# Optimization experiments

Measured on AMD Instinct MI355X. Metric: run time of the kernel, lower is better.

Reference implementation:

```python
import jax, jax.numpy as jnp
import numpy as np

B, L, C, H, W = 4, 8, 32, 128, 256
M1, M2 = 32, 32  # spectral modes


def setup_inputs() -> dict:
    key = jax.random.key(0)
    k1, k2, k3, k4, k5, k6 = jax.random.split(key, 6)
    scale = 1.0 / (C * C)
    return {
        "x": jax.random.normal(k1, (B, L, C, H, W), dtype=jnp.float32),
        "k": jax.random.normal(k2, (C, H, W), dtype=jnp.float32),
        "w1r": scale * jax.random.normal(k3, (C, C, M1, M2), dtype=jnp.float32),
        "w1i": scale * jax.random.normal(k4, (C, C, M1, M2), dtype=jnp.float32),
        "w2r": scale * jax.random.normal(k5, (C, C, M1, M2), dtype=jnp.float32),
        "w2i": scale * jax.random.normal(k6, (C, C, M1, M2), dtype=jnp.float32),
    }


def reference(x, k, w1r, w1i, w2r, w2i):
    # x: [B, L, C, H, W] real; k: [C, H, W] conv kernel (broadcast over B*L).
    b, l, c, h, w = x.shape
    # --- FlashFFTConvInterface fallback path: circular conv via rfft2.
    # H, W are already 2/3/5-smooth (next_fast_len is identity -> no padding).
    u = x.reshape(b * l, c, h, w)
    u_f = jnp.fft.rfft2(u)                     # [B*L, C, H, W//2+1] complex
    k_f = jnp.fft.rfft2(k)                     # [C, H, W//2+1], broadcasts
    y = jnp.fft.irfft2(u_f * k_f, s=(h, w)).reshape(b, l, c, h, w)

    # --- SpectralConv2d: per-mode channel mixing in frequency domain.
    x_f = jnp.fft.rfft2(y)                     # [B, L, C, H, Wf] complex
    wf = x_f.shape[-1]
    w1 = (w1r + 1j * w1i).astype(x_f.dtype)
    w2 = (w2r + 1j * w2i).astype(x_f.dtype)
    m1 = min(h, M1)
    m2 = min(wf, M2)
    co = w1.shape[1]
    top = jnp.einsum('blcij,coij->bloij', x_f[:, :, :, :m1, :m2], w1[:, :, :m1, :m2])
    out_f = jnp.zeros((b, l, co, h, wf), dtype=x_f.dtype)
    out_f = out_f.at[:, :, :, :m1, :m2].set(top)
    if h > 1 and (h > M1 or wf > M2):
        bot = jnp.einsum('blcij,coij->bloij', x_f[:, :, :, h - m1:, :m2], w2[:, :, :m1, :m2])
        out_f = out_f.at[:, :, :, h - m1:, :m2].set(bot)
    return jnp.fft.irfft2(out_f, s=(h, w))    # [B, L, Co, H, W] real
```

## Files before the change

kernel.cpp:

```cpp
#include <hip/hip_runtime.h>
#include <math.h>

#define Hn 128
#define Wn 256
#define PLANE (Hn*Wn)

#define OFF_TQC 0u
#define OFF_TQS 2048u
#define OFF_TP  4096u
#define OFF_KM  16384u
#define OFF_XM  147456u
#define OFF_B   4341760u
#define OFF_RK  12730368u

__global__ __launch_bounds__(256) void build_tables(float* __restrict__ ws) {
  int tid = blockIdx.x * 256 + threadIdx.x;
  const double PI2 = 6.283185307179586476925286766559;
  if (tid < 512) {
    int j = tid >> 4, xi = tid & 15;
    float cc[4], ss[4];
#pragma unroll
    for (int m = 0; m < 4; m++) {
      int x = xi * 4 + m;
      double ang = PI2 * (double)((j * x) & 255) / 256.0;
      cc[m] = (float)cos(ang); ss[m] = (float)sin(ang);
    }
    ((float4*)(ws + OFF_TQC))[tid] = make_float4(cc[0], cc[1], cc[2], cc[3]);
    ((float4*)(ws + OFF_TQS))[tid] = make_float4(ss[0], ss[1], ss[2], ss[3]);
  }
  if (tid < 2048) {
    int p = tid >> 6, y2 = tid & 63;
    double a0 = PI2 * (double)((p * (2 * y2)) & 127) / 128.0;
    double a1 = PI2 * (double)((p * (2 * y2 + 1)) & 127) / 128.0;
    ((float4*)(ws + OFF_TP))[tid] =
        make_float4((float)cos(a0), (float)sin(a0), (float)cos(a1), (float)sin(a1));
  }
}

#define RS 276
__global__ __launch_bounds__(256, 3) void fwd_rows(const float* __restrict__ src,
                                                   float2* __restrict__ R,
                                                   const float* __restrict__ ws) {
  int plane = blockIdx.x >> 2, chunk = blockIdx.x & 3;
  __shared__ __align__(16) float Sd[32 * RS];
  __shared__ float4 Tc[544], Ts[544];
  int t = threadIdx.x;
  const float4* src4 = (const float4*)src;
  size_t sb = (size_t)plane * 8192 + (size_t)chunk * 2048;
#pragma unroll
  for (int k = 0; k < 8; k++) {
    int idx = t + 256 * k;
    int row = idx >> 6, c4 = idx & 63;
    int sws = (row >> 1) & 15;
    *(float4*)&Sd[row * RS + ((c4 ^ sws) << 2)] = src4[sb + idx];
  }
  const float4* gTc = (const float4*)(ws + OFF_TQC);
  const float4* gTs = (const float4*)(ws + OFF_TQS);
#pragma unroll
  for (int k = 0; k < 2; k++) {
    int idx = t + 256 * k;
    Tc[(idx >> 4) * 17 + (idx & 15)] = gTc[idx];
    Ts[(idx >> 4) * 17 + (idx & 15)] = gTs[idx];
  }
  __syncthreads();
  float EPv[2][4], EMv[2][4], OPv[2][4], OMv[2][4];
  float spE64[2], spU128[2], spO64[2];
#pragma unroll
  for (int uu = 0; uu < 2; uu++) {
    int unit = uu * 256 + t;
    int y = unit >> 4, xq = unit & 15;
    int sws = (y >> 1) & 15;
    const float* rowp = &Sd[y * RS];
    float4 A0 = *(const float4*)&rowp[(xq ^ sws) << 2];
    float4 A2 = *(const float4*)&rowp[((32 + xq) ^ sws) << 2];
    float Av0[4] = {A0.x, A0.y, A0.z, A0.w};
    float Av2[4] = {A2.x, A2.y, A2.z, A2.w};
    float M1[4], M2[4];
#pragma unroll
    for (int kk = 0; kk < 4; kk++) {
      int s1 = 128 - 4 * xq - kk;
      M1[kk] = rowp[(((s1 >> 2) ^ sws) << 2) + (s1 & 3)];
      int s2 = 256 - 4 * xq - kk;
      int s2c = (s2 > 255) ? 255 : s2;
      M2[kk] = rowp[(((s2c >> 2) ^ sws) << 2) + (s2c & 3)];
    }
#pragma unroll
    for (int kk = 0; kk < 4; kk++) {
      float a = Av0[kk] + M2[kk], b = Av0[kk] - M2[kk];
      float c = M1[kk] + Av2[kk], d = M1[kk] - Av2[kk];
      EPv[uu][kk] = a + c;  EMv[uu][kk] = a - c;
      OPv[uu][kk] = b + d;  OMv[uu][kk] = b - d;
    }
    spE64[uu] = 0.f; spU128[uu] = 0.f; spO64[uu] = 0.f;
    if (xq == 0) {
      EPv[uu][0] = Av0[0];  EMv[uu][0] = Av0[0];
      OPv[uu][0] = 0.f;     OMv[uu][0] = 0.f;
      float u64v  = rowp[((16 ^ sws) << 2)];
      float u192v = rowp[((48 ^ sws) << 2)];
      spE64[uu]  = u64v + u192v;
      spO64[uu]  = u64v - u192v;
      spU128[uu] = Av2[0];
    }
  }
  __syncthreads();
#pragma unroll
  for (int uu = 0; uu < 2; uu++) {
    int unit = uu * 256 + t;
    int y = unit >> 4, xq = unit & 15;
    int sws = (y >> 1) & 15;
    float* rowp = &Sd[y * RS];
    int off = (xq ^ sws) << 2;
    *(float4*)&rowp[off]       = make_float4(EPv[uu][0], EPv[uu][1], EPv[uu][2], EPv[uu][3]);
    *(float4*)&rowp[68 + off]  = make_float4(EMv[uu][0], EMv[uu][1], EMv[uu][2], EMv[uu][3]);
    *(float4*)&rowp[136 + off] = make_float4(OMv[uu][0], OMv[uu][1], OMv[uu][2], OMv[uu][3]);
    *(float4*)&rowp[204 + off] = make_float4(OPv[uu][0], OPv[uu][1], OPv[uu][2], OPv[uu][3]);
    if (xq == 0) {
      rowp[64] = spE64[uu];
      rowp[65] = spU128[uu];
      rowp[66] = spO64[uu];
    }
  }
  __syncthreads();
  int jg = t & 15, yg = t >> 4;
  int jodd = jg & 1;
  int aC = jodd ? 68 : 0;
  int aS = jodd ? 204 : 136;
  const float4* pC0 = &Tc[jg * 17];
  const float4* pS0 = &Ts[jg * 17];
  const float4* pC1 = &Tc[(jg + 16) * 17];
  const float4* pS1 = &Ts[(jg + 16) * 17];
  float sgE = jodd ? 0.f : (((jg >> 1) & 1) ? -1.f : 1.f);
  float sgO = jodd ? ((((jg - 1) >> 1) & 1) ? -1.f : 1.f) : 0.f;
  float pm = jodd ? -1.f : 1.f;
  int sw = yg;
  const float* row0 = &Sd[(2 * yg) * RS];
  const float* row1 = &Sd[(2 * yg + 1) * RS];
  float dc[2][2], dsn[2][2];
#pragma unroll
  for (int a = 0; a < 2; a++)
#pragma unroll
    for (int b = 0; b < 2; b++) { dc[a][b] = 0.f; dsn[a][b] = 0.f; }
#define DOT4(a, b) (a.x * b.x + a.y * b.y + a.z * b.z + a.w * b.w)
#pragma unroll 4
  for (int xb = 0; xb < 16; xb++) {
    int off = (xb ^ sw) << 2;
    float4 eY0 = *(const float4*)&row0[aC + off];
    float4 eY1 = *(const float4*)&row1[aC + off];
    float4 oY0 = *(const float4*)&row0[aS + off];
    float4 oY1 = *(const float4*)&row1[aS + off];
    float4 c0 = pC0[xb], s0 = pS0[xb];
    float4 c1 = pC1[xb], s1 = pS1[xb];
    dc[0][0] += DOT4(eY0, c0);  dc[0][1] += DOT4(eY1, c0);
    dc[1][0] += DOT4(eY0, c1);  dc[1][1] += DOT4(eY1, c1);
    dsn[0][0] += DOT4(oY0, s0); dsn[0][1] += DOT4(oY1, s0);
    dsn[1][0] += DOT4(oY0, s1); dsn[1][1] += DOT4(oY1, s1);
  }
#undef DOT4
  float E64_0 = row0[64], u128_0 = row0[65], O64_0 = row0[66];
  float E64_1 = row1[64], u128_1 = row1[65], O64_1 = row1[66];
#pragma unroll
  for (int jj = 0; jj < 2; jj++) {
    int j = jg + 16 * jj;
#pragma unroll
    for (int ky = 0; ky < 2; ky++) {
      int y = chunk * 32 + yg * 2 + ky;
      float E64 = ky ? E64_1 : E64_0;
      float u128 = ky ? u128_1 : u128_0;
      float O64 = ky ? O64_1 : O64_0;
      float re = dc[jj][ky] + sgE * E64 + pm * u128;
      float im = -dsn[jj][ky] - sgO * O64;
      R[((size_t)plane * 128 + y) * 32 + j] = make_float2(re, im);
    }
  }
}
#undef RS

__global__ __launch_bounds__(256) void fwd_cols(const float2* __restrict__ Rg,
                                                float2* __restrict__ dst,
                                                const float* __restrict__ ws) {
  int plane = blockIdx.x;
  __shared__ float4 Rs4[2048];
  __shared__ float4 TPs[2048];
  float2* Rs = (float2*)Rs4;
  int t = threadIdx.x;
  const float4* in4 = (const float4*)(Rg + (size_t)plane * 4096);
#pragma unroll
  for (int k = 0; k < 8; k++) Rs4[t + 256 * k] = in4[t + 256 * k];
  const float4* gTP = (const float4*)(ws + OFF_TP);
#pragma unroll
  for (int k = 0; k < 8; k++) TPs[t + 256 * k] = gTP[t + 256 * k];
  __syncthreads();
  int j = t & 31, pg = t >> 5;
  float Are[4], Aim[4], Bre[4], Bim[4];
#pragma unroll
  for (int m = 0; m < 4; m++) { Are[m] = Aim[m] = Bre[m] = Bim[m] = 0.f; }
  for (int it = 0; it < 32; it++) {
#pragma unroll
    for (int h = 0; h < 2; h++) {
      int y2 = 2 * it + h;
      float sg = (h == 0) ? 1.f : -1.f;
      float2 r0 = Rs[(2 * y2) * 32 + j];
      float2 r1 = Rs[(2 * y2 + 1) * 32 + j];
#pragma unroll
      for (int m = 0; m < 4; m++) {
        int p = pg + 8 * m;
        float4 tw = TPs[p * 64 + y2];
        float P0 = r0.x * tw.x + r0.y * tw.y;
        float Q0 = r0.y * tw.x - r0.x * tw.y;
        float P1 = r1.x * tw.z + r1.y * tw.w;
        float Q1 = r1.y * tw.z - r1.x * tw.w;
        Are[m] += P0 + P1;
        Aim[m] += Q0 + Q1;
        Bre[m] += sg * (P0 - Q1);
        Bim[m] += sg * (Q0 + P1);
      }
    }
  }
  size_t ob = (size_t)plane * 2048;
#pragma unroll
  for (int m = 0; m < 4; m++) {
    int p = pg + 8 * m;
    dst[ob + p * 32 + j] = make_float2(Are[m], Aim[m]);
    dst[ob + (32 + p) * 32 + j] = make_float2(Bre[m], Bim[m]);
  }
}

__global__ __launch_bounds__(256) void wk_build(const float* __restrict__ w1r,
                                                const float* __restrict__ w1i,
                                                const float* __restrict__ w2r,
                                                const float* __restrict__ w2i,
                                                float2* __restrict__ wk,
                                                const float2* __restrict__ km) {
  int e0 = blockIdx.x * 256 + threadIdx.x;
#pragma unroll
  for (int k = 0; k < 4; k++) {
    int e = e0 + k * 524288;
    int o = e & 31, c = (e >> 5) & 31, j = (e >> 10) & 31, i64 = e >> 15;
    int r = (i64 < 32) ? i64 : i64 - 32;
    const float* wr = (i64 < 32) ? w1r : w2r;
    const float* wi = (i64 < 32) ? w1i : w2i;
    int widx = ((c * 32 + o) * 32 + r) * 32 + j;
    float wrv = wr[widx], wiv = wi[widx];
    float2 kv = km[(size_t)c * 2048 + i64 * 32 + j];
    wk[e] = make_float2(kv.x * wrv - kv.y * wiv, kv.x * wiv + kv.y * wrv);
  }
}

__global__ __launch_bounds__(256) void mix_modes(float2* __restrict__ xm,
                                                 const float2* __restrict__ wk) {
  int bid = blockIdx.x;
  int mode = (bid & 7) * 256 + (bid >> 3);
  __shared__ float4 Xs4[512], Ws4[512];
  float2* Xs = (float2*)Xs4;
  float2* Wsl = (float2*)Ws4;
  int t = threadIdx.x;
#pragma unroll
  for (int k = 0; k < 4; k++) {
    int p = t + 256 * k;
    Xs[p] = xm[(size_t)p * 2048 + mode];
  }
  const float4* wk4 = (const float4*)(wk + (size_t)mode * 1024);
#pragma unroll
  for (int k = 0; k < 2; k++) Ws4[t + 256 * k] = wk4[t + 256 * k];
  __syncthreads();
  int o = t & 31, bg = t >> 5;
  float orr[4], oii[4];
#pragma unroll
  for (int m = 0; m < 4; m++) { orr[m] = 0.f; oii[m] = 0.f; }
  for (int c2 = 0; c2 < 16; c2++) {
    float2 w0 = Wsl[(2 * c2) * 32 + o];
    float2 w1 = Wsl[(2 * c2 + 1) * 32 + o];
#pragma unroll
    for (int m = 0; m < 4; m++) {
      float4 xv = *(const float4*)&Xs[(bg * 4 + m) * 32 + 2 * c2];
      orr[m] += xv.x * w0.x - xv.y * w0.y + xv.z * w1.x - xv.w * w1.y;
      oii[m] += xv.x * w0.y + xv.y * w0.x + xv.z * w1.y + xv.w * w1.x;
    }
  }
#pragma unroll
  for (int m = 0; m < 4; m++)
    xm[(size_t)((bg * 4 + m) * 32 + o) * 2048 + mode] = make_float2(orr[m], oii[m]);
}

__global__ __launch_bounds__(256) void inv_rows(const float2* __restrict__ om,
                                                float2* __restrict__ G,
                                                const float* __restrict__ ws) {
  int plane = blockIdx.x;
  __shared__ float4 Os4[1024];
  __shared__ float4 TPs[2048];
  float2* Os = (float2*)Os4;
  int t = threadIdx.x;
  const float4* in4 = (const float4*)(om + (size_t)plane * 2048);
#pragma unroll
  for (int k = 0; k < 4; k++) Os4[t + 256 * k] = in4[t + 256 * k];
  const float4* gTP = (const float4*)(ws + OFF_TP);
#pragma unroll
  for (int k = 0; k < 8; k++) TPs[t + 256 * k] = gTP[t + 256 * k];
  __syncthreads();
  int j = t & 31, yg = t >> 5;
  float gr[16], gi[16];
#pragma unroll
  for (int k = 0; k < 16; k++) { gr[k] = 0.f; gi[k] = 0.f; }
  for (int p = 0; p < 32; p++) {
    float2 A = Os[p * 32 + j];
    float2 B = Os[(32 + p) * 32 + j];
#pragma unroll
    for (int mp = 0; mp < 8; mp++) {
      int y2 = yg * 8 + mp;
      float4 tw = TPs[p * 64 + y2];
      float sg = ((mp & 1) == 0) ? 1.f : -1.f;
      float Sr = A.x + sg * B.x, Si = A.y + sg * B.y;
      gr[2 * mp]     += Sr * tw.x - Si * tw.y;
      gi[2 * mp]     += Sr * tw.y + Si * tw.x;
      float Tr = A.x + sg * B.y, Ti = A.y - sg * B.x;
      gr[2 * mp + 1] += Tr * tw.z - Ti * tw.w;
      gi[2 * mp + 1] += Tr * tw.w + Ti * tw.z;
    }
  }
  const float inv = 1.0f / 32768.0f;
  size_t gb = (size_t)plane * 128;
#pragma unroll
  for (int mm = 0; mm < 16; mm++) {
    int y = yg * 16 + mm;
    float sr = (j == 0) ? gr[mm] * inv : 2.f * inv * gr[mm];
    float si = (j == 0) ? 0.f : 2.f * inv * gi[mm];
    G[(gb + y) * 32 + j] = make_float2(sr, si);
  }
}

__global__ __launch_bounds__(256) void inv_cols(const float2* __restrict__ G,
                                                float* __restrict__ out,
                                                const float* __restrict__ ws) {
  int plane = blockIdx.x >> 2, chunk = blockIdx.x & 3;
  __shared__ float2 Gs[32 * 33];
  __shared__ float4 Tc[544], Ts[544];
  int t = threadIdx.x;
  const float2* in = G + (size_t)plane * 4096 + (size_t)chunk * 1024;
#pragma unroll
  for (int k = 0; k < 4; k++) {
    int idx = t + 256 * k;
    Gs[(idx >> 5) * 33 + (idx & 31)] = in[idx];
  }
  const float4* gTc = (const float4*)(ws + OFF_TQC);
  const float4* gTs = (const float4*)(ws + OFF_TQS);
#pragma unroll
  for (int k = 0; k < 2; k++) {
    int idx = t + 256 * k;
    Tc[(idx >> 4) * 17 + (idx & 15)] = gTc[idx];
    Ts[(idx >> 4) * 17 + (idx & 15)] = gTs[idx];
  }
  __syncthreads();
  int xi = t & 15, yg = t >> 4;
  float4 Ce[2], Co[2], Se[2], So[2];
  float c64[2], s64[2];
#pragma unroll
  for (int ky = 0; ky < 2; ky++) {
    Ce[ky] = make_float4(0.f, 0.f, 0.f, 0.f);
    Co[ky] = make_float4(0.f, 0.f, 0.f, 0.f);
    Se[ky] = make_float4(0.f, 0.f, 0.f, 0.f);
    So[ky] = make_float4(0.f, 0.f, 0.f, 0.f);
    c64[ky] = 0.f; s64[ky] = 0.f;
  }
#define FMA4(acc, s, v) do { acc.x += (s) * (v).x; acc.y += (s) * (v).y; \
                             acc.z += (s) * (v).z; acc.w += (s) * (v).w; } while (0)
#pragma unroll 4
  for (int jh = 0; jh < 16; jh++) {
    float4 ce = Tc[(2 * jh) * 17 + xi],     se = Ts[(2 * jh) * 17 + xi];
    float4 co = Tc[(2 * jh + 1) * 17 + xi], so = Ts[(2 * jh + 1) * 17 + xi];
    float sgn = (jh & 1) ? -1.f : 1.f;
#pragma unroll
    for (int ky = 0; ky < 2; ky++) {
      float2 ge = Gs[(yg * 2 + ky) * 33 + 2 * jh];
      float2 go = Gs[(yg * 2 + ky) * 33 + 2 * jh + 1];
      FMA4(Ce[ky], ge.x, ce);
      FMA4(Se[ky], ge.y, se);
      FMA4(Co[ky], go.x, co);
      FMA4(So[ky], go.y, so);
      c64[ky] += sgn * ge.x;
      s64[ky] += sgn * go.y;
    }
  }
#undef FMA4
  float* outp = out + (size_t)plane * PLANE + (size_t)chunk * 32 * Wn;
#pragma unroll
  for (int ky = 0; ky < 2; ky++) {
    int y = yg * 2 + ky;
    float* ro = outp + y * Wn;
    float4 C  = make_float4(Ce[ky].x + Co[ky].x, Ce[ky].y + Co[ky].y,
                            Ce[ky].z + Co[ky].z, Ce[ky].w + Co[ky].w);
    float4 Cm = make_float4(Ce[ky].x - Co[ky].x, Ce[ky].y - Co[ky].y,
                            Ce[ky].z - Co[ky].z, Ce[ky].w - Co[ky].w);
    float4 S  = make_float4(Se[ky].x + So[ky].x, Se[ky].y + So[ky].y,
                            Se[ky].z + So[ky].z, Se[ky].w + So[ky].w);
    float4 Sm = make_float4(So[ky].x - Se[ky].x, So[ky].y - Se[ky].y,
                            So[ky].z - Se[ky].z, So[ky].w - Se[ky].w);
    *(float4*)(ro + 4 * xi) =
        make_float4(C.x - S.x, C.y - S.y, C.z - S.z, C.w - S.w);
    *(float4*)(ro + 128 + 4 * xi) =
        make_float4(Cm.x + Sm.x, Cm.y + Sm.y, Cm.z + Sm.z, Cm.w + Sm.w);
    int mb = 128 - 4 * xi;
    ro[mb]     = Cm.x - Sm.x;
    ro[mb - 1] = Cm.y - Sm.y;
    ro[mb - 2] = Cm.z - Sm.z;
    ro[mb - 3] = Cm.w - Sm.w;
    int nb = 256 - 4 * xi;
    if (xi) ro[nb] = C.x + S.x;
    ro[nb - 1] = C.y + S.y;
    ro[nb - 2] = C.z + S.z;
    ro[nb - 3] = C.w + S.w;
    if (xi == 0) {
      ro[64]  = c64[ky] - s64[ky];
      ro[192] = c64[ky] + s64[ky];
    }
  }
}

extern "C" void kernel_launch(void* const* d_in, const int* in_sizes, int n_in,
                              void* d_out, int out_size, void* d_ws, size_t ws_size,
                              hipStream_t stream) {
  (void)in_sizes; (void)n_in; (void)out_size; (void)ws_size;
  const float* x   = (const float*)d_in[0];
  const float* kk  = (const float*)d_in[1];
  const float* w1r = (const float*)d_in[2];
  const float* w1i = (const float*)d_in[3];
  const float* w2r = (const float*)d_in[4];
  const float* w2i = (const float*)d_in[5];
  float*  ws   = (float*)d_ws;
  float*  out  = (float*)d_out;
  float2* km2  = (float2*)(ws + OFF_KM);
  float2* xm2  = (float2*)(ws + OFF_XM);
  float2* bx   = (float2*)(ws + OFF_B);
  float2* rk   = (float2*)(ws + OFF_RK);

  build_tables<<<8, 256, 0, stream>>>(ws);
  fwd_rows<<<4096, 256, 0, stream>>>(x, bx, ws);
  fwd_rows<<<128, 256, 0, stream>>>(kk, rk, ws);
  fwd_cols<<<1024, 256, 0, stream>>>(bx, xm2, ws);
  fwd_cols<<<32, 256, 0, stream>>>(rk, km2, ws);
  wk_build<<<2048, 256, 0, stream>>>(w1r, w1i, w2r, w2i, bx, km2);
  mix_modes<<<2048, 256, 0, stream>>>(xm2, bx);
  inv_rows<<<1024, 256, 0, stream>>>(xm2, bx, ws);
  inv_cols<<<4096, 256, 0, stream>>>(bx, out, ws);
}
```

Measured before the change: 417.9 us.

## Fuse row and column DFT passes into single per-plane forward and inverse kernels

Merges fwd_rows+fwd_cols into one kernel per plane that loops over four row chunks and keeps the 128x32 row-spectrum in LDS, and likewise fuses inv_rows+inv_cols keeping the intermediate in LDS. This removes the global round-trip of intermediate spectra and two launches per direction. Twiddle tables are now read from global/cache instead of staged in LDS, and grids shrink to one block per plane (1024 blocks) with lower occupancy target, which reduces parallelism and may raise latency.

```diff
diff --git a/kernel.cpp b/kernel.cpp
--- a/kernel.cpp
+++ b/kernel.cpp
@@ -38,154 +38,139 @@
 }
 
 #define RS 276
-__global__ __launch_bounds__(256, 3) void fwd_rows(const float* __restrict__ src,
-                                                   float2* __restrict__ R,
-                                                   const float* __restrict__ ws) {
-  int plane = blockIdx.x >> 2, chunk = blockIdx.x & 3;
-  __shared__ __align__(16) float Sd[32 * RS];
-  __shared__ float4 Tc[544], Ts[544];
+__global__ __launch_bounds__(256, 2) void fwd_fused(const float* __restrict__ src,
+                                                    float2* __restrict__ dst,
+                                                    const float* __restrict__ ws) {
+  int plane = blockIdx.x;
+  __shared__ __align__(16) float U[32 * RS];
+  __shared__ __align__(16) float2 RL[128 * 33];
   int t = threadIdx.x;
   const float4* src4 = (const float4*)src;
-  size_t sb = (size_t)plane * 8192 + (size_t)chunk * 2048;
-#pragma unroll
-  for (int k = 0; k < 8; k++) {
-    int idx = t + 256 * k;
-    int row = idx >> 6, c4 = idx & 63;
-    int sws = (row >> 1) & 15;
-    *(float4*)&Sd[row * RS + ((c4 ^ sws) << 2)] = src4[sb + idx];
-  }
+  size_t sb = (size_t)plane * 8192;
   const float4* gTc = (const float4*)(ws + OFF_TQC);
   const float4* gTs = (const float4*)(ws + OFF_TQS);
-#pragma unroll
-  for (int k = 0; k < 2; k++) {
-    int idx = t + 256 * k;
-    Tc[(idx >> 4) * 17 + (idx & 15)] = gTc[idx];
-    Ts[(idx >> 4) * 17 + (idx & 15)] = gTs[idx];
-  }
-  __syncthreads();
-  float EPv[2][4], EMv[2][4], OPv[2][4], OMv[2][4];
-  float spE64[2], spU128[2], spO64[2];
-#pragma unroll
-  for (int uu = 0; uu < 2; uu++) {
-    int unit = uu * 256 + t;
-    int y = unit >> 4, xq = unit & 15;
-    int sws = (y >> 1) & 15;
-    const float* rowp = &Sd[y * RS];
-    float4 A0 = *(const float4*)&rowp[(xq ^ sws) << 2];
-    float4 A2 = *(const float4*)&rowp[((32 + xq) ^ sws) << 2];
-    float Av0[4] = {A0.x, A0.y, A0.z, A0.w};
-    float Av2[4] = {A2.x, A2.y, A2.z, A2.w};
-    float M1[4], M2[4];
-#pragma unroll
-    for (int kk = 0; kk < 4; kk++) {
-      int s1 = 128 - 4 * xq - kk;
-      M1[kk] = rowp[(((s1 >> 2) ^ sws) << 2) + (s1 & 3)];
-      int s2 = 256 - 4 * xq - kk;
-      int s2c = (s2 > 255) ? 255 : s2;
-      M2[kk] = rowp[(((s2c >> 2) ^ sws) << 2) + (s2c & 3)];
-    }
-#pragma unroll
-    for (int kk = 0; kk < 4; kk++) {
-      float a = Av0[kk] + M2[kk], b = Av0[kk] - M2[kk];
-      float c = M1[kk] + Av2[kk], d = M1[kk] - Av2[kk];
-      EPv[uu][kk] = a + c;  EMv[uu][kk] = a - c;
-      OPv[uu][kk] = b + d;  OMv[uu][kk] = b - d;
-    }
-    spE64[uu] = 0.f; spU128[uu] = 0.f; spO64[uu] = 0.f;
-    if (xq == 0) {
-      EPv[uu][0] = Av0[0];  EMv[uu][0] = Av0[0];
-      OPv[uu][0] = 0.f;     OMv[uu][0] = 0.f;
-      float u64v  = rowp[((16 ^ sws) << 2)];
-      float u192v = rowp[((48 ^ sws) << 2)];
-      spE64[uu]  = u64v + u192v;
-      spO64[uu]  = u64v - u192v;
-      spU128[uu] = Av2[0];
-    }
-  }
-  __syncthreads();
-#pragma unroll
-  for (int uu = 0; uu < 2; uu++) {
-    int unit = uu * 256 + t;
-    int y = unit >> 4, xq = unit & 15;
-    int sws = (y >> 1) & 15;
-    float* rowp = &Sd[y * RS];
-    int off = (xq ^ sws) << 2;
-    *(float4*)&rowp[off]       = make_float4(EPv[uu][0], EPv[uu][1], EPv[uu][2], EPv[uu][3]);
-    *(float4*)&rowp[68 + off]  = make_float4(EMv[uu][0], EMv[uu][1], EMv[uu][2], EMv[uu][3]);
-    *(float4*)&rowp[136 + off] = make_float4(OMv[uu][0], OMv[uu][1], OMv[uu][2], OMv[uu][3]);
-    *(float4*)&rowp[204 + off] = make_float4(OPv[uu][0], OPv[uu][1], OPv[uu][2], OPv[uu][3]);
-    if (xq == 0) {
-      rowp[64] = spE64[uu];
-      rowp[65] = spU128[uu];
-      rowp[66] = spO64[uu];
-    }
-  }
-  __syncthreads();
+
   int jg = t & 15, yg = t >> 4;
   int jodd = jg & 1;
   int aC = jodd ? 68 : 0;
   int aS = jodd ? 204 : 136;
-  const float4* pC0 = &Tc[jg * 17];
-  const float4* pS0 = &Ts[jg * 17];
-  const float4* pC1 = &Tc[(jg + 16) * 17];
-  const float4* pS1 = &Ts[(jg + 16) * 17];
+  const float4* pC0 = gTc + jg * 16;
+  const float4* pS0 = gTs + jg * 16;
+  const float4* pC1 = gTc + (jg + 16) * 16;
+  const float4* pS1 = gTs + (jg + 16) * 16;
   float sgE = jodd ? 0.f : (((jg >> 1) & 1) ? -1.f : 1.f);
   float sgO = jodd ? ((((jg - 1) >> 1) & 1) ? -1.f : 1.f) : 0.f;
   float pm = jodd ? -1.f : 1.f;
   int sw = yg;
-  const float* row0 = &Sd[(2 * yg) * RS];
-  const float* row1 = &Sd[(2 * yg + 1) * RS];
-  float dc[2][2], dsn[2][2];
-#pragma unroll
-  for (int a = 0; a < 2; a++)
-#pragma unroll
-    for (int b = 0; b < 2; b++) { dc[a][b] = 0.f; dsn[a][b] = 0.f; }
+
+  for (int ch = 0; ch < 4; ch++) {
+#pragma unroll
+    for (int k = 0; k < 8; k++) {
+      int idx = t + 256 * k;
+      int row = idx >> 6, c4 = idx & 63;
+      int sws = (row >> 1) & 15;
+      *(float4*)&U[row * RS + ((c4 ^ sws) << 2)] = src4[sb + ch * 2048 + idx];
+    }
+    __syncthreads();
+    float EPv[2][4], EMv[2][4], OPv[2][4], OMv[2][4];
+    float spE64[2], spU128[2], spO64[2];
+#pragma unroll
+    for (int uu = 0; uu < 2; uu++) {
+      int unit = uu * 256 + t;
+      int y = unit >> 4, xq = unit & 15;
+      int sws = (y >> 1) & 15;
+      const float* rowp = &U[y * RS];
+      float4 A0 = *(const float4*)&rowp[(xq ^ sws) << 2];
+      float4 A2 = *(const float4*)&rowp[((32 + xq) ^ sws) << 2];
+      float Av0[4] = {A0.x, A0.y, A0.z, A0.w};
+      float Av2[4] = {A2.x, A2.y, A2.z, A2.w};
+      float M1[4], M2[4];
+#pragma unroll
+      for (int kk = 0; kk < 4; kk++) {
+        int s1 = 128 - 4 * xq - kk;
+        M1[kk] = rowp[(((s1 >> 2) ^ sws) << 2) + (s1 & 3)];
+        int s2 = 256 - 4 * xq - kk;
+        int s2c = (s2 > 255) ? 255 : s2;
+        M2[kk] = rowp[(((s2c >> 2) ^ sws) << 2) + (s2c & 3)];
+      }
+#pragma unroll
+      for (int kk = 0; kk < 4; kk++) {
+        float a = Av0[kk] + M2[kk], b = Av0[kk] - M2[kk];
+        float c = M1[kk] + Av2[kk], d = M1[kk] - Av2[kk];
+        EPv[uu][kk] = a + c;  EMv[uu][kk] = a - c;
+        OPv[uu][kk] = b + d;  OMv[uu][kk] = b - d;
+      }
+      spE64[uu] = 0.f; spU128[uu] = 0.f; spO64[uu] = 0.f;
+      if (xq == 0) {
+        EPv[uu][0] = Av0[0];  EMv[uu][0] = Av0[0];
+        OPv[uu][0] = 0.f;     OMv[uu][0] = 0.f;
+        float u64v  = rowp[((16 ^ sws) << 2)];
+        float u192v = rowp[((48 ^ sws) << 2)];
+        spE64[uu]  = u64v + u192v;
+        spO64[uu]  = u64v - u192v;
+        spU128[uu] = Av2[0];
+      }
+    }
+    __syncthreads();
+#pragma unroll
+    for (int uu = 0; uu < 2; uu++) {
+      int unit = uu * 256 + t;
+      int y = unit >> 4, xq = unit & 15;
+      int sws = (y >> 1) & 15;
+      float* rowp = &U[y * RS];
+      int off = (xq ^ sws) << 2;
+      *(float4*)&rowp[off]       = make_float4(EPv[uu][0], EPv[uu][1], EPv[uu][2], EPv[uu][3]);
+      *(float4*)&rowp[68 + off]  = make_float4(EMv[uu][0], EMv[uu][1], EMv[uu][2], EMv[uu][3]);
+      *(float4*)&rowp[136 + off] = make_float4(OMv[uu][0], OMv[uu][1], OMv[uu][2], OMv[uu][3]);
+      *(float4*)&rowp[204 + off] = make_float4(OPv[uu][0], OPv[uu][1], OPv[uu][2], OPv[uu][3]);
+      if (xq == 0) {
+        rowp[64] = spE64[uu];
+        rowp[65] = spU128[uu];
+        rowp[66] = spO64[uu];
+      }
+    }
+    __syncthreads();
+    const float* row0 = &U[(2 * yg) * RS];
+    const float* row1 = &U[(2 * yg + 1) * RS];
+    float dc[2][2], dsn[2][2];
+#pragma unroll
+    for (int a = 0; a < 2; a++)
+#pragma unroll
+      for (int b = 0; b < 2; b++) { dc[a][b] = 0.f; dsn[a][b] = 0.f; }
 #define DOT4(a, b) (a.x * b.x + a.y * b.y + a.z * b.z + a.w * b.w)
 #pragma unroll 4
-  for (int xb = 0; xb < 16; xb++) {
-    int off = (xb ^ sw) << 2;
-    float4 eY0 = *(const float4*)&row0[aC + off];
-    float4 eY1 = *(const float4*)&row1[aC + off];
-    float4 oY0 = *(const float4*)&row0[aS + off];
-    float4 oY1 = *(const float4*)&row1[aS + off];
-    float4 c0 = pC0[xb], s0 = pS0[xb];
-    float4 c1 = pC1[xb], s1 = pS1[xb];
-    dc[0][0] += DOT4(eY0, c0);  dc[0][1] += DOT4(eY1, c0);
-    dc[1][0] += DOT4(eY0, c1);  dc[1][1] += DOT4(eY1, c1);
-    dsn[0][0] += DOT4(oY0, s0); dsn[0][1] += DOT4(oY1, s0);
-    dsn[1][0] += DOT4(oY0, s1); dsn[1][1] += DOT4(oY1, s1);
-  }
+    for (int xb = 0; xb < 16; xb++) {
+      int off = (xb ^ sw) << 2;
+      float4 eY0 = *(const float4*)&row0[aC + off];
+      float4 eY1 = *(const float4*)&row1[aC + off];
+      float4 oY0 = *(const float4*)&row0[aS + off];
+      float4 oY1 = *(const float4*)&row1[aS + off];
+      float4 c0 = pC0[xb], s0 = pS0[xb];
+      float4 c1 = pC1[xb], s1 = pS1[xb];
+      dc[0][0] += DOT4(eY0, c0);  dc[0][1] += DOT4(eY1, c0);
+      dc[1][0] += DOT4(eY0, c1);  dc[1][1] += DOT4(eY1, c1);
+      dsn[0][0] += DOT4(oY0, s0); dsn[0][1] += DOT4(oY1, s0);
+      dsn[1][0] += DOT4(oY0, s1); dsn[1][1] += DOT4(oY1, s1);
+    }
 #undef DOT4
-  float E64_0 = row0[64], u128_0 = row0[65], O64_0 = row0[66];
-  float E64_1 = row1[64], u128_1 = row1[65], O64_1 = row1[66];
-#pragma unroll
-  for (int jj = 0; jj < 2; jj++) {
-    int j = jg + 16 * jj;
-#pragma unroll
-    for (int ky = 0; ky < 2; ky++) {
-      int y = chunk * 32 + yg * 2 + ky;
-      float E64 = ky ? E64_1 : E64_0;
-      float u128 = ky ? u128_1 : u128_0;
-      float O64 = ky ? O64_1 : O64_0;
-      float re = dc[jj][ky] + sgE * E64 + pm * u128;
-      float im = -dsn[jj][ky] - sgO * O64;
-      R[((size_t)plane * 128 + y) * 32 + j] = make_float2(re, im);
-    }
-  }
-}
-#undef RS
-
-__global__ __launch_bounds__(256) void fwd_cols(const float2* __restrict__ Rg,
-                                                float2* __restrict__ dst,
-                                                const float* __restrict__ ws) {
-  int plane = blockIdx.x;
-  __shared__ float4 Rs4[2048];
-  __shared__ float4 TPs[2048];
-  float2* Rs = (float2*)Rs4;
-  int t = threadIdx.x;
-  const float4* in4 = (const float4*)(Rg + (size_t)plane * 4096);
-#pragma unroll
-  for (int k = 0; k < 8; k++) Rs4[t + 256 * k] = in4[t + 256 * k];
+    float E64_0 = row0[64], u128_0 = row0[65], O64_0 = row0[66];
+    float E64_1 = row1[64], u128_1 = row1[65], O64_1 = row1[66];
+#pragma unroll
+    for (int jj = 0; jj < 2; jj++) {
+#pragma unroll
+      for (int ky = 0; ky < 2; ky++) {
+        float E64 = ky ? E64_1 : E64_0;
+        float u128 = ky ? u128_1 : u128_0;
+        float O64 = ky ? O64_1 : O64_0;
+        float re = dc[jj][ky] + sgE * E64 + pm * u128;
+        float im = -dsn[jj][ky] - sgO * O64;
+        RL[(ch * 32 + yg * 2 + ky) * 33 + (jg + 16 * jj)] = make_float2(re, im);
+      }
+    }
+    __syncthreads();
+  }
+
+  float4* TPs = (float4*)U;
   const float4* gTP = (const float4*)(ws + OFF_TP);
 #pragma unroll
   for (int k = 0; k < 8; k++) TPs[t + 256 * k] = gTP[t + 256 * k];
@@ -199,8 +184,8 @@
     for (int h = 0; h < 2; h++) {
       int y2 = 2 * it + h;
       float sg = (h == 0) ? 1.f : -1.f;
-      float2 r0 = Rs[(2 * y2) * 32 + j];
-      float2 r1 = Rs[(2 * y2 + 1) * 32 + j];
+      float2 r0 = RL[(2 * y2) * 33 + j];
+      float2 r1 = RL[(2 * y2 + 1) * 33 + j];
 #pragma unroll
       for (int m = 0; m < 4; m++) {
         int p = pg + 8 * m;
@@ -224,6 +209,7 @@
     dst[ob + (32 + p) * 32 + j] = make_float2(Bre[m], Bim[m]);
   }
 }
+#undef RS
 
 __global__ __launch_bounds__(256) void wk_build(const float* __restrict__ w1r,
                                                 const float* __restrict__ w1i,
@@ -282,135 +268,115 @@
     xm[(size_t)((bg * 4 + m) * 32 + o) * 2048 + mode] = make_float2(orr[m], oii[m]);
 }
 
-__global__ __launch_bounds__(256) void inv_rows(const float2* __restrict__ om,
-                                                float2* __restrict__ G,
-                                                const float* __restrict__ ws) {
+__global__ __launch_bounds__(256, 2) void inv_fused(const float2* __restrict__ om,
+                                                    float* __restrict__ out,
+                                                    const float* __restrict__ ws) {
   int plane = blockIdx.x;
-  __shared__ float4 Os4[1024];
-  __shared__ float4 TPs[2048];
-  float2* Os = (float2*)Os4;
+  __shared__ __align__(16) float4 TPs[2048];
+  __shared__ __align__(16) float2 GL[128 * 33];
   int t = threadIdx.x;
-  const float4* in4 = (const float4*)(om + (size_t)plane * 2048);
-#pragma unroll
-  for (int k = 0; k < 4; k++) Os4[t + 256 * k] = in4[t + 256 * k];
   const float4* gTP = (const float4*)(ws + OFF_TP);
 #pragma unroll
   for (int k = 0; k < 8; k++) TPs[t + 256 * k] = gTP[t + 256 * k];
   __syncthreads();
-  int j = t & 31, yg = t >> 5;
-  float gr[16], gi[16];
-#pragma unroll
-  for (int k = 0; k < 16; k++) { gr[k] = 0.f; gi[k] = 0.f; }
-  for (int p = 0; p < 32; p++) {
-    float2 A = Os[p * 32 + j];
-    float2 B = Os[(32 + p) * 32 + j];
-#pragma unroll
-    for (int mp = 0; mp < 8; mp++) {
-      int y2 = yg * 8 + mp;
-      float4 tw = TPs[p * 64 + y2];
-      float sg = ((mp & 1) == 0) ? 1.f : -1.f;
-      float Sr = A.x + sg * B.x, Si = A.y + sg * B.y;
-      gr[2 * mp]     += Sr * tw.x - Si * tw.y;
-      gi[2 * mp]     += Sr * tw.y + Si * tw.x;
-      float Tr = A.x + sg * B.y, Ti = A.y - sg * B.x;
-      gr[2 * mp + 1] += Tr * tw.z - Ti * tw.w;
-      gi[2 * mp + 1] += Tr * tw.w + Ti * tw.z;
-    }
-  }
-  const float inv = 1.0f / 32768.0f;
-  size_t gb = (size_t)plane * 128;
-#pragma unroll
-  for (int mm = 0; mm < 16; mm++) {
-    int y = yg * 16 + mm;
-    float sr = (j == 0) ? gr[mm] * inv : 2.f * inv * gr[mm];
-    float si = (j == 0) ? 0.f : 2.f * inv * gi[mm];
-    G[(gb + y) * 32 + j] = make_float2(sr, si);
-  }
-}
-
-__global__ __launch_bounds__(256) void inv_cols(const float2* __restrict__ G,
-                                                float* __restrict__ out,
-                                                const float* __restrict__ ws) {
-  int plane = blockIdx.x >> 2, chunk = blockIdx.x & 3;
-  __shared__ float2 Gs[32 * 33];
-  __shared__ float4 Tc[544], Ts[544];
-  int t = threadIdx.x;
-  const float2* in = G + (size_t)plane * 4096 + (size_t)chunk * 1024;
-#pragma unroll
-  for (int k = 0; k < 4; k++) {
-    int idx = t + 256 * k;
-    Gs[(idx >> 5) * 33 + (idx & 31)] = in[idx];
-  }
+  {
+    int j = t & 31, yg = t >> 5;
+    const float2* omp = om + (size_t)plane * 2048;
+    float gr[16], gi[16];
+#pragma unroll
+    for (int k = 0; k < 16; k++) { gr[k] = 0.f; gi[k] = 0.f; }
+    for (int p = 0; p < 32; p++) {
+      float2 A = omp[p * 32 + j];
+      float2 B = omp[(32 + p) * 32 + j];
+#pragma unroll
+      for (int mp = 0; mp < 8; mp++) {
+        int y2 = yg * 8 + mp;
+        float4 tw = TPs[p * 64 + y2];
+        float sg = ((mp & 1) == 0) ? 1.f : -1.f;
+        float Sr = A.x + sg * B.x, Si = A.y + sg * B.y;
+        gr[2 * mp]     += Sr * tw.x - Si * tw.y;
+        gi[2 * mp]     += Sr * tw.y + Si * tw.x;
+        float Tr = A.x + sg * B.y, Ti = A.y - sg * B.x;
+        gr[2 * mp + 1] += Tr * tw.z - Ti * tw.w;
+        gi[2 * mp + 1] += Tr * tw.w + Ti * tw.z;
+      }
+    }
+    const float inv = 1.0f / 32768.0f;
+#pragma unroll
+    for (int mm = 0; mm < 16; mm++) {
+      int y = yg * 16 + mm;
+      float sr = (j == 0) ? gr[mm] * inv : 2.f * inv * gr[mm];
+      float si = (j == 0) ? 0.f : 2.f * inv * gi[mm];
+      GL[y * 33 + j] = make_float2(sr, si);
+    }
+  }
+  __syncthreads();
   const float4* gTc = (const float4*)(ws + OFF_TQC);
   const float4* gTs = (const float4*)(ws + OFF_TQS);
-#pragma unroll
-  for (int k = 0; k < 2; k++) {
-    int idx = t + 256 * k;
-    Tc[(idx >> 4) * 17 + (idx & 15)] = gTc[idx];
-    Ts[(idx >> 4) * 17 + (idx & 15)] = gTs[idx];
-  }
-  __syncthreads();
   int xi = t & 15, yg = t >> 4;
-  float4 Ce[2], Co[2], Se[2], So[2];
-  float c64[2], s64[2];
-#pragma unroll
-  for (int ky = 0; ky < 2; ky++) {
-    Ce[ky] = make_float4(0.f, 0.f, 0.f, 0.f);
-    Co[ky] = make_float4(0.f, 0.f, 0.f, 0.f);
-    Se[ky] = make_float4(0.f, 0.f, 0.f, 0.f);
-    So[ky] = make_float4(0.f, 0.f, 0.f, 0.f);
-    c64[ky] = 0.f; s64[ky] = 0.f;
-  }
+  for (int ch = 0; ch < 4; ch++) {
+    float4 Ce[2], Co[2], Se[2], So[2];
+    float c64[2], s64[2];
+#pragma unroll
+    for (int ky = 0; ky < 2; ky++) {
+      Ce[ky] = make_float4(0.f, 0.f, 0.f, 0.f);
+      Co[ky] = make_float4(0.f, 0.f, 0.f, 0.f);
+      Se[ky] = make_float4(0.f, 0.f, 0.f, 0.f);
+      So[ky] = make_float4(0.f, 0.f, 0.f, 0.f);
+      c64[ky] = 0.f; s64[ky] = 0.f;
+    }
 #define FMA4(acc, s, v) do { acc.x += (s) * (v).x; acc.y += (s) * (v).y; \
                              acc.z += (s) * (v).z; acc.w += (s) * (v).w; } while (0)
 #pragma unroll 4
-  for (int jh = 0; jh < 16; jh++) {
-    float4 ce = Tc[(2 * jh) * 17 + xi],     se = Ts[(2 * jh) * 17 + xi];
-    float4 co = Tc[(2 * jh + 1) * 17 + xi], so = Ts[(2 * jh + 1) * 17 + xi];
-    float sgn = (jh & 1) ? -1.f : 1.f;
+    for (int jh = 0; jh < 16; jh++) {
+      float4 ce = gTc[(2 * jh) * 16 + xi],     se = gTs[(2 * jh) * 16 + xi];
+      float4 co = gTc[(2 * jh + 1) * 16 + xi], so = gTs[(2 * jh + 1) * 16 + xi];
+      float sgn = (jh & 1) ? -1.f : 1.f;
+#pragma unroll
+      for (int ky = 0; ky < 2; ky++) {
+        int y = ch * 32 + yg * 2 + ky;
+        float2 ge = GL[y * 33 + 2 * jh];
+        float2 go = GL[y * 33 + 2 * jh + 1];
+        FMA4(Ce[ky], ge.x, ce);
+        FMA4(Se[ky], ge.y, se);
+        FMA4(Co[ky], go.x, co);
+        FMA4(So[ky], go.y, so);
+        c64[ky] += sgn * ge.x;
+        s64[ky] += sgn * go.y;
+      }
+    }
+#undef FMA4
+    float* outp = out + (size_t)plane * PLANE + (size_t)ch * 32 * Wn;
 #pragma unroll
     for (int ky = 0; ky < 2; ky++) {
-      float2 ge = Gs[(yg * 2 + ky) * 33 + 2 * jh];
-      float2 go = Gs[(yg * 2 + ky) * 33 + 2 * jh + 1];
-      FMA4(Ce[ky], ge.x, ce);
-      FMA4(Se[ky], ge.y, se);
-      FMA4(Co[ky], go.x, co);
-      FMA4(So[ky], go.y, so);
-      c64[ky] += sgn * ge.x;
-      s64[ky] += sgn * go.y;
-    }
-  }
-#undef FMA4
-  float* outp = out + (size_t)plane * PLANE + (size_t)chunk * 32 * Wn;
-#pragma unroll
-  for (int ky = 0; ky < 2; ky++) {
-    int y = yg * 2 + ky;
-    float* ro = outp + y * Wn;
-    float4 C  = make_float4(Ce[ky].x + Co[ky].x, Ce[ky].y + Co[ky].y,
-                            Ce[ky].z + Co[ky].z, Ce[ky].w + Co[ky].w);
-    float4 Cm = make_float4(Ce[ky].x - Co[ky].x, Ce[ky].y - Co[ky].y,
-                            Ce[ky].z - Co[ky].z, Ce[ky].w - Co[ky].w);
-    float4 S  = make_float4(Se[ky].x + So[ky].x, Se[ky].y + So[ky].y,
-                            Se[ky].z + So[ky].z, Se[ky].w + So[ky].w);
-    float4 Sm = make_float4(So[ky].x - Se[ky].x, So[ky].y - Se[ky].y,
-                            So[ky].z - Se[ky].z, So[ky].w - Se[ky].w);
-    *(float4*)(ro + 4 * xi) =
-        make_float4(C.x - S.x, C.y - S.y, C.z - S.z, C.w - S.w);
-    *(float4*)(ro + 128 + 4 * xi) =
-        make_float4(Cm.x + Sm.x, Cm.y + Sm.y, Cm.z + Sm.z, Cm.w + Sm.w);
-    int mb = 128 - 4 * xi;
-    ro[mb]     = Cm.x - Sm.x;
-    ro[mb - 1] = Cm.y - Sm.y;
-    ro[mb - 2] = Cm.z - Sm.z;
-    ro[mb - 3] = Cm.w - Sm.w;
-    int nb = 256 - 4 * xi;
-    if (xi) ro[nb] = C.x + S.x;
-    ro[nb - 1] = C.y + S.y;
-    ro[nb - 2] = C.z + S.z;
-    ro[nb - 3] = C.w + S.w;
-    if (xi == 0) {
-      ro[64]  = c64[ky] - s64[ky];
-      ro[192] = c64[ky] + s64[ky];
+      int y = yg * 2 + ky;
+      float* ro = outp + y * Wn;
+      float4 C  = make_float4(Ce[ky].x + Co[ky].x, Ce[ky].y + Co[ky].y,
+                              Ce[ky].z + Co[ky].z, Ce[ky].w + Co[ky].w);
+      float4 Cm = make_float4(Ce[ky].x - Co[ky].x, Ce[ky].y - Co[ky].y,
+                              Ce[ky].z - Co[ky].z, Ce[ky].w - Co[ky].w);
+      float4 S  = make_float4(Se[ky].x + So[ky].x, Se[ky].y + So[ky].y,
+                              Se[ky].z + So[ky].z, Se[ky].w + So[ky].w);
+      float4 Sm = make_float4(So[ky].x - Se[ky].x, So[ky].y - Se[ky].y,
+                              So[ky].z - Se[ky].z, So[ky].w - Se[ky].w);
+      *(float4*)(ro + 4 * xi) =
+          make_float4(C.x - S.x, C.y - S.y, C.z - S.z, C.w - S.w);
+      *(float4*)(ro + 128 + 4 * xi) =
+          make_float4(Cm.x + Sm.x, Cm.y + Sm.y, Cm.z + Sm.z, Cm.w + Sm.w);
+      int mb = 128 - 4 * xi;
+      ro[mb]     = Cm.x - Sm.x;
+      ro[mb - 1] = Cm.y - Sm.y;
+      ro[mb - 2] = Cm.z - Sm.z;
+      ro[mb - 3] = Cm.w - Sm.w;
+      int nb = 256 - 4 * xi;
+      if (xi) ro[nb] = C.x + S.x;
+      ro[nb - 1] = C.y + S.y;
+      ro[nb - 2] = C.z + S.z;
+      ro[nb - 3] = C.w + S.w;
+      if (xi == 0) {
+        ro[64]  = c64[ky] - s64[ky];
+        ro[192] = c64[ky] + s64[ky];
+      }
     }
   }
 }
@@ -429,16 +395,12 @@
   float*  out  = (float*)d_out;
   float2* km2  = (float2*)(ws + OFF_KM);
   float2* xm2  = (float2*)(ws + OFF_XM);
-  float2* bx   = (float2*)(ws + OFF_B);
-  float2* rk   = (float2*)(ws + OFF_RK);
+  float2* wk2  = (float2*)(ws + OFF_B);
 
   build_tables<<<8, 256, 0, stream>>>(ws);
-  fwd_rows<<<4096, 256, 0, stream>>>(x, bx, ws);
-  fwd_rows<<<128, 256, 0, stream>>>(kk, rk, ws);
-  fwd_cols<<<1024, 256, 0, stream>>>(bx, xm2, ws);
-  fwd_cols<<<32, 256, 0, stream>>>(rk, km2, ws);
-  wk_build<<<2048, 256, 0, stream>>>(w1r, w1i, w2r, w2i, bx, km2);
-  mix_modes<<<2048, 256, 0, stream>>>(xm2, bx);
-  inv_rows<<<1024, 256, 0, stream>>>(xm2, bx, ws);
-  inv_cols<<<4096, 256, 0, stream>>>(bx, out, ws);
-}
+  fwd_fused<<<1024, 256, 0, stream>>>(x, xm2, ws);
+  fwd_fused<<<32, 256, 0, stream>>>(kk, km2, ws);
+  wk_build<<<2048, 256, 0, stream>>>(w1r, w1i, w2r, w2i, wk2, km2);
+  mix_modes<<<2048, 256, 0, stream>>>(xm2, wk2);
+  inv_fused<<<1024, 256, 0, stream>>>(xm2, out, ws);
+}
```

Result: slower. 538.6 us (+28.9%).
